# Optimization experiments

Hardware: AMD Instinct MI355X
Metric: run time of the kernel (lower is better)

Reference implementation:

```python
import jax, jax.numpy as jnp
import numpy as np

DIM = 768
NUM_HEADS = 12
HEAD_DIM = DIM // NUM_HEADS
B, N = 16, 784


def setup_inputs() -> dict:
    key = jax.random.key(0)
    k1, k2, k3, k4, k5 = jax.random.split(key, 5)
    x = jax.random.normal(k1, (B, N, DIM), dtype=jnp.float32)
    # Dense params (flax Dense: kernel [in, out], bias [out])
    Wqkv = jax.random.normal(k2, (DIM, 3 * DIM), dtype=jnp.float32) * (DIM ** -0.5)
    bqkv = jnp.zeros((3 * DIM,), dtype=jnp.float32)
    Wo = jax.random.normal(k3, (DIM, DIM), dtype=jnp.float32) * (DIM ** -0.5)
    bo = jnp.zeros((DIM,), dtype=jnp.float32)
    return {"x": x, "Wqkv": Wqkv, "bqkv": bqkv, "Wo": Wo, "bo": bo}


def reference(x, Wqkv, bqkv, Wo, bo):
    b, n, dim = x.shape
    # fused QKV projection
    qkv = jnp.einsum('bnd,df->bnf', x, Wqkv) + bqkv          # [b, n, 3*dim]
    qkv = qkv.reshape(b, n, 3, NUM_HEADS, HEAD_DIM)           # '(k h d)' split
    q, k, v = qkv[:, :, 0], qkv[:, :, 1], qkv[:, :, 2]        # [b, n, h, d]
    scale = HEAD_DIM ** -0.5
    # chunked/flash path computes exact softmax attention; same math, expressed densely
    scores = jnp.einsum('bihd,bjhd->bhij', q, k) * scale      # [b, h, n, n]
    attn = jax.nn.softmax(scores, axis=-1)
    out = jnp.einsum('bhij,bjhd->bihd', attn, v)              # [b, n, h, d]
    out = out.reshape(b, n, dim)                              # 'b n (h d)'
    return jnp.einsum('bnd,df->bnf', out, Wo) + bo
```

## Files before the change

kernel.cpp:

```cpp
#include <hip/hip_runtime.h>

#define DIM 768
#define NHEADS 12
#define HDIM 64
#define BB 16
#define NN 784
#define M_TOTAL (BB * NN)

typedef __attribute__((ext_vector_type(8))) _Float16 f16x8;
typedef __attribute__((ext_vector_type(4))) float f32x4;
typedef __attribute__((ext_vector_type(16))) float f32x16;
typedef __fp16 fp16x2 __attribute__((ext_vector_type(2)));

typedef __attribute__((address_space(3))) unsigned int lds_uint;
typedef __attribute__((address_space(1))) const unsigned int g_uint;
__device__ inline void gload_lds16(const void* g, void* l) {
    __builtin_amdgcn_global_load_lds((g_uint*)(uintptr_t)g,
                                     (lds_uint*)(uintptr_t)l, 16, 0, 0);
}

#if __has_builtin(__builtin_amdgcn_exp2f)
#define EXP2(x) __builtin_amdgcn_exp2f(x)
#else
#define EXP2(x) exp2f(x)
#endif

__device__ inline unsigned int pk2(float a, float b, float* lacc) {
#if __has_builtin(__builtin_amdgcn_cvt_pkrtz)
    union { fp16x2 h; unsigned int u; } r;
    r.h = __builtin_amdgcn_cvt_pkrtz(a, b);
#if __has_builtin(__builtin_amdgcn_fdot2)
    const fp16x2 one = {(__fp16)1.f, (__fp16)1.f};
    *lacc = __builtin_amdgcn_fdot2(r.h, one, *lacc, false);
#else
    *lacc += a + b;
#endif
    return r.u;
#else
    union { _Float16 h[2]; unsigned int u; } r;
    r.h[0] = (_Float16)a; r.h[1] = (_Float16)b;
    *lacc += a + b;
    return r.u;
#endif
}

__global__ __launch_bounds__(256) void prep_kernel(
    const float* __restrict__ x, _Float16* __restrict__ xh,
    const float* __restrict__ Wqkv, _Float16* __restrict__ wqT,
    const float* __restrict__ Wo, _Float16* __restrict__ woT)
{
    const int NC  = (M_TOTAL * DIM) / (8 * 256);
    const int NQX = (3 * DIM) / 32;
    const int NQ  = NQX * (DIM / 32);
    const int NOX = DIM / 32;
    const int bid = blockIdx.x;

    if (bid < NC) {
        const int i = (bid * 256 + threadIdx.x) * 8;
        float4 a = *(const float4*)&x[i];
        float4 b = *(const float4*)&x[i + 4];
        union { _Float16 h[8]; uint4 v; } o;
        o.h[0] = (_Float16)a.x; o.h[1] = (_Float16)a.y;
        o.h[2] = (_Float16)a.z; o.h[3] = (_Float16)a.w;
        o.h[4] = (_Float16)b.x; o.h[5] = (_Float16)b.y;
        o.h[6] = (_Float16)b.z; o.h[7] = (_Float16)b.w;
        *(uint4*)&xh[i] = o.v;
        return;
    }

    __shared__ float t[32][33];
    const float* W; _Float16* T; int N, n0, k0;
    if (bid < NC + NQ) {
        const int lb = bid - NC;
        W = Wqkv; T = wqT; N = 3 * DIM;
        n0 = (lb % NQX) * 32; k0 = (lb / NQX) * 32;
    } else {
        const int lb = bid - NC - NQ;
        W = Wo; T = woT; N = DIM;
        n0 = (lb % NOX) * 32; k0 = (lb / NOX) * 32;
    }
    const int K = DIM;
    const int r = threadIdx.x >> 3, c4 = (threadIdx.x & 7) * 4;
    float4 v = *(const float4*)&W[(size_t)(k0 + r) * N + n0 + c4];
    t[r][c4 + 0] = v.x; t[r][c4 + 1] = v.y;
    t[r][c4 + 2] = v.z; t[r][c4 + 3] = v.w;
    __syncthreads();
    union { _Float16 h[4]; ushort4 v4; } o;
#pragma unroll
    for (int i = 0; i < 4; ++i) o.h[i] = (_Float16)t[c4 + i][r];
    *(ushort4*)&T[(size_t)(n0 + r) * K + k0 + c4] = o.v4;
}

#define G_STAGE(BUF, K0)                                                       \
  {                                                                            \
    _Pragma("unroll")                                                          \
    for (int i = 0; i < 4; ++i) {                                              \
        const int rbase = w * 32 + i * 8;                                      \
        gload_lds16(A + (size_t)(gm + rbase + srow) * K + (K0) + scol,         \
                    &sA[BUF][rbase * 64]);                                     \
        gload_lds16(B + (size_t)(gn + rbase + srow) * K + (K0) + scol,         \
                    &sB[BUF][rbase * 64]);                                     \
    }                                                                          \
  }

#define G_COMPUTE(BUF)                                                         \
  {                                                                            \
    _Pragma("unroll")                                                          \
    for (int kk = 0; kk < 4; ++kk) {                                           \
        const int c = kk * 2 + hi;                                             \
        const int sw = (c ^ (l31 & 7)) * 8;                                    \
        f16x8 a[4], bb[2];                                                     \
        _Pragma("unroll")                                                      \
        for (int mt = 0; mt < 4; ++mt)                                         \
            a[mt] = *(const f16x8*)&sA[BUF][(wm + mt * 32 + l31) * 64 + sw];   \
        _Pragma("unroll")                                                      \
        for (int nt = 0; nt < 2; ++nt)                                         \
            bb[nt] = *(const f16x8*)&sB[BUF][(wn + nt * 32 + l31) * 64 + sw];  \
        __builtin_amdgcn_s_setprio(1);                                         \
        _Pragma("unroll")                                                      \
        for (int mt = 0; mt < 4; ++mt)                                         \
            _Pragma("unroll")                                                  \
            for (int nt = 0; nt < 2; ++nt)                                     \
                acc[mt][nt] = __builtin_amdgcn_mfma_f32_32x32x16_f16(          \
                    a[mt], bb[nt], acc[mt][nt], 0, 0, 0);                      \
        __builtin_amdgcn_s_setprio(0);                                         \
    }                                                                          \
  }

template <int OUT_F16>
__global__ __launch_bounds__(512) void gemm_f16_kernel(
    const _Float16* __restrict__ A, const _Float16* __restrict__ B,
    const float* __restrict__ bias, void* __restrict__ Cout,
    int M, int N, int K)
{
    __shared__ _Float16 sA[2][256 * 64];
    __shared__ _Float16 sB[2][256 * 64];

    const int tid  = threadIdx.x;
    const int w    = tid >> 6;
    const int lane = tid & 63;

    const int nwg = gridDim.x * gridDim.y;
    const int lid = blockIdx.x + gridDim.x * blockIdx.y;
    const int cq  = nwg >> 3, cr = nwg & 7;
    const int xcd = lid & 7, ix = lid >> 3;
    const int wgid = (xcd < cr ? xcd * (cq + 1) : cr * (cq + 1) + (xcd - cr) * cq) + ix;
    const int gn = (wgid % gridDim.x) * 256;
    const int gm = (wgid / gridDim.x) * 256;

    const int wm = (w & 1) * 128;
    const int wn = (w >> 1) * 64;
    const int l31 = lane & 31;
    const int hi  = lane >> 5;

    const int srow = lane >> 3;
    const int scol = ((lane & 7) ^ srow) * 8;

    f32x16 acc[4][2] = {};

    const int NT = K >> 6;
    G_STAGE(0, 0)
    __syncthreads();
    int cur = 0;
#pragma unroll 1
    for (int t = 0; t < NT - 1; ++t) {
        G_STAGE(cur ^ 1, (t + 1) * 64)
        G_COMPUTE(cur)
        __syncthreads();
        cur ^= 1;
    }
    G_COMPUTE(cur)

#pragma unroll
    for (int nt = 0; nt < 2; ++nt) {
        const int col = gn + wn + nt * 32 + l31;
        const float bv = bias[col];
#pragma unroll
        for (int mt = 0; mt < 4; ++mt) {
            f32x16 v = acc[mt][nt];
#pragma unroll
            for (int reg = 0; reg < 16; ++reg) {
                const int row = gm + wm + mt * 32 + (reg & 3) + 8 * (reg >> 2) + 4 * hi;
                const float o = v[reg] + bv;
                if (OUT_F16)
                    ((_Float16*)Cout)[(size_t)row * N + col] = (_Float16)o;
                else
                    ((float*)Cout)[(size_t)row * N + col] = o;
            }
        }
    }
}

#define LOG2E_8 0.18033688f

#define LOAD_TILE(J0, TAIL)                                                    \
  {                                                                            \
    const int j0_ = (J0);                                                      \
    int jrowK = j0_ + sj;                                                      \
    if (TAIL && jrowK > NN - 1) jrowK = NN - 1;                                \
    const size_t kbase = (size_t)(b * NN + jrowK) * (3 * DIM) + DIM + h * HDIM;\
    k0v = *(const uint4*)&qkv[kbase + sg * 8];                                 \
    k1v = *(const uint4*)&qkv[kbase + sg * 8 + 32];                            \
    int vr0 = j0_ + 2 * jj, vr1 = j0_ + 2 * jj + 1;                            \
    if (TAIL) { if (vr0 > NN - 1) vr0 = NN - 1; if (vr1 > NN - 1) vr1 = NN - 1; } \
    va.v = *(const uint4*)&qkv[(size_t)(b * NN + vr0) * (3 * DIM) + 2 * DIM + h * HDIM + dsub]; \
    vc.v = *(const uint4*)&qkv[(size_t)(b * NN + vr1) * (3 * DIM) + 2 * DIM + h * HDIM + dsub]; \
  }

#define WRITE_TILE(BUF)                                                        \
  {                                                                            \
    _Float16 (*K_)[72] = Ks[BUF];                                              \
    _Float16 (*V_)[72] = Vt[BUF];                                              \
    *(uint4*)&K_[sj][sg * 8]      = k0v;                                       \
    *(uint4*)&K_[sj][sg * 8 + 32] = k1v;                                       \
    _Pragma("unroll")                                                          \
    for (int i = 0; i < 8; ++i) {                                              \
        union { _Float16 h2[2]; unsigned int u; } t;                           \
        t.h2[0] = va.h[i]; t.h2[1] = vc.h[i];                                  \
        *(unsigned int*)&V_[dsub + i][pcol] = t.u;                             \
    }                                                                          \
  }

#define EXP_PACK(SV, G, J0_, TAIL)                                             \
  {                                                                            \
    float p0 = EXP2(SV[0]), p1 = EXP2(SV[1]);                                  \
    float p2 = EXP2(SV[2]), p3 = EXP2(SV[3]);                                  \
    if (TAIL && (J0_ + nt * 16) >= NN) { p0 = p1 = p2 = p3 = 0.f; }            \
    pk[G][nt][0] = pk2(p0, p1, &lpart[G]);                                     \
    pk[G][nt][1] = pk2(p2, p3, &lpart[G]);                                     \
  }

#define COMPUTE_TILE(BUF, J0, TAIL)                                            \
  {                                                                            \
    _Float16 (*K_)[72] = Ks[BUF];                                              \
    _Float16 (*V_)[72] = Vt[BUF];                                              \
    unsigned int pk[2][4][2];                                                  \
    _Pragma("unroll")                                                          \
    for (int nt = 0; nt < 4; ++nt) {                                           \
        f16x8 kf0 = *(const f16x8*)&K_[nt * 16 + l16][quad * 8];               \
        f16x8 kf1 = *(const f16x8*)&K_[nt * 16 + l16][32 + quad * 8];          \
        f32x4 s0 = {}, s1 = {};                                                \
        s0 = __builtin_amdgcn_mfma_f32_16x16x32_f16(kf0, qfrag[0][0], s0, 0, 0, 0); \
        s0 = __builtin_amdgcn_mfma_f32_16x16x32_f16(kf1, qfrag[0][1], s0, 0, 0, 0); \
        s1 = __builtin_amdgcn_mfma_f32_16x16x32_f16(kf0, qfrag[1][0], s1, 0, 0, 0); \
        s1 = __builtin_amdgcn_mfma_f32_16x16x32_f16(kf1, qfrag[1][1], s1, 0, 0, 0); \
        EXP_PACK(s0, 0, J0, TAIL)                                              \
        EXP_PACK(s1, 1, J0, TAIL)                                              \
    }                                                                          \
    __builtin_amdgcn_s_setprio(1);                                             \
    _Pragma("unroll")                                                          \
    for (int pc = 0; pc < 2; ++pc) {                                           \
        union { unsigned int u[4]; f16x8 v; } pa0, pa1;                        \
        pa0.u[0] = pk[0][2 * pc][0];     pa0.u[1] = pk[0][2 * pc][1];          \
        pa0.u[2] = pk[0][2 * pc + 1][0]; pa0.u[3] = pk[0][2 * pc + 1][1];      \
        pa1.u[0] = pk[1][2 * pc][0];     pa1.u[1] = pk[1][2 * pc][1];          \
        pa1.u[2] = pk[1][2 * pc + 1][0]; pa1.u[3] = pk[1][2 * pc + 1][1];      \
        _Pragma("unroll")                                                      \
        for (int dt = 0; dt < 4; ++dt) {                                       \
            f16x8 vf = *(const f16x8*)&V_[dt * 16 + l16][pc * 32 + quad * 8];  \
            O[0][dt] = __builtin_amdgcn_mfma_f32_16x16x32_f16(pa0.v, vf, O[0][dt], 0, 0, 0); \
            O[1][dt] = __builtin_amdgcn_mfma_f32_16x16x32_f16(pa1.v, vf, O[1][dt], 0, 0, 0); \
        }                                                                      \
    }                                                                          \
    __builtin_amdgcn_s_setprio(0);                                             \
  }

__global__ __launch_bounds__(256, 2) void attn_f16_kernel(
    const _Float16* __restrict__ qkv, _Float16* __restrict__ oat)
{
    const int L   = blockIdx.x + 7 * (blockIdx.y + NHEADS * blockIdx.z);
    const int xcd = L & 7, ixc = L >> 3;
    const int grp = xcd * 24 + ixc / 7;
    const int q0  = (ixc % 7) * 128;
    const int b   = grp / NHEADS;
    const int h   = grp % NHEADS;

    const int tid = threadIdx.x;
    const int wave = tid >> 6;
    const int lane = tid & 63;
    const int quad = lane >> 4;
    const int l16  = lane & 15;

    __shared__ _Float16 Ks[2][64][72];
    __shared__ _Float16 Vt[2][64][72];

    f16x8 qfrag[2][2];
#pragma unroll
    for (int g = 0; g < 2; ++g) {
        int qrow = q0 + wave * 32 + g * 16 + l16; if (qrow > NN - 1) qrow = NN - 1;
        size_t base = (size_t)(b * NN + qrow) * (3 * DIM) + h * HDIM;
        qfrag[g][0] = (*(const f16x8*)&qkv[base + quad * 8]) * (_Float16)LOG2E_8;
        qfrag[g][1] = (*(const f16x8*)&qkv[base + 32 + quad * 8]) * (_Float16)LOG2E_8;
    }

    const int sj = lane;
    const int sg = wave;
    const int jj   = lane & 31;
    const int dsub = sg * 16 + (lane >> 5) * 8;
    const int pcol = ((jj >> 4) << 5) | (((jj >> 1) & 3) << 3)
                   | (((jj >> 3) & 1) << 2) | ((jj & 1) << 1);

    f32x4 O[2][4] = {};
    float lpart[2] = {0.f, 0.f};

    uint4 k0v, k1v;
    union { uint4 v; _Float16 h[8]; } va, vc;

    LOAD_TILE(0, 0)
#pragma unroll 1
    for (int jt = 0; jt < 11; ++jt) {
        WRITE_TILE(jt & 1)
        __syncthreads();
        LOAD_TILE((jt + 1) * 64, 0)
        COMPUTE_TILE(jt & 1, 0, 0)
    }
    WRITE_TILE(1)
    __syncthreads();
    LOAD_TILE(768, 1)
    COMPUTE_TILE(1, 704, 0)
    WRITE_TILE(0)
    __syncthreads();
    COMPUTE_TILE(0, 768, 1)

#pragma unroll
    for (int g = 0; g < 2; ++g) {
        float t = lpart[g];
        t += __shfl_xor(t, 16);
        t += __shfl_xor(t, 32);
        float inv[4];
#pragma unroll
        for (int r = 0; r < 4; ++r)
            inv[r] = 1.0f / __shfl(t, quad * 4 + r, 16);
#pragma unroll
        for (int r = 0; r < 4; ++r) {
            const int q = q0 + wave * 32 + g * 16 + quad * 4 + r;
            if (q < NN) {
#pragma unroll
                for (int dt = 0; dt < 4; ++dt) {
                    const size_t base = (size_t)(b * NN + q) * DIM + h * HDIM + dt * 16 + l16;
                    oat[base] = (_Float16)(O[g][dt][r] * inv[r]);
                }
            }
        }
    }
}

extern "C" void kernel_launch(void* const* d_in, const int* in_sizes, int n_in,
                              void* d_out, int out_size, void* d_ws, size_t ws_size,
                              hipStream_t stream) {
    const float* x    = (const float*)d_in[0];
    const float* Wqkv = (const float*)d_in[1];
    const float* bqkv = (const float*)d_in[2];
    const float* Wo   = (const float*)d_in[3];
    const float* bo   = (const float*)d_in[4];
    float* out = (float*)d_out;

    _Float16* qkv = (_Float16*)d_ws;
    _Float16* xh  = qkv + (size_t)M_TOTAL * 3 * DIM;
    _Float16* wqT = xh + (size_t)M_TOTAL * DIM;
    _Float16* woT = wqT + (size_t)3 * DIM * DIM;
    _Float16* oat = xh;

    {
        const int NC = (M_TOTAL * DIM) / (8 * 256);
        const int NQ = ((3 * DIM) / 32) * (DIM / 32);
        const int NO_ = (DIM / 32) * (DIM / 32);
        prep_kernel<<<NC + NQ + NO_, 256, 0, stream>>>(
            x, xh, Wqkv, wqT, Wo, woT);
    }
    gemm_f16_kernel<1><<<dim3((3 * DIM) / 256, M_TOTAL / 256), 512, 0, stream>>>(
        xh, wqT, bqkv, qkv, M_TOTAL, 3 * DIM, DIM);
    attn_f16_kernel<<<dim3(7, NHEADS, BB), 256, 0, stream>>>(qkv, oat);
    gemm_f16_kernel<0><<<dim3(DIM / 256, M_TOTAL / 256), 512, 0, stream>>>(
        oat, woT, bo, out, M_TOTAL, DIM, DIM);
}
```

Before: 228.3 us.

## Interleave global-to-LDS loads with MFMA phases using fine-grained vmcnt waits

Restructures the double-buffered GEMM main loop so the next tile's B and A loads are issued in chunks between four MFMA phases. Each phase covers one 32-row A subtile, and explicit s_waitcnt vmcnt counts plus raw s_barrier replace __syncthreads. B fragments are held in registers across the whole k-tile and A is read per phase. The aim is to spread memory issue and hide load latency under matrix math. In exchange it carries more live registers and depends on fragile manual wait counts and buffer-reuse ordering, which could race.

New measurement: 226.0 us, median of 2. No clear change (-1.0%).

```diff
diff --git a/kernel.cpp b/kernel.cpp
--- a/kernel.cpp
+++ b/kernel.cpp
@@ -91,41 +91,43 @@
     *(ushort4*)&T[(size_t)(n0 + r) * K + k0 + c4] = o.v4;
 }
 
-#define G_STAGE(BUF, K0)                                                       \
-  {                                                                            \
-    _Pragma("unroll")                                                          \
-    for (int i = 0; i < 4; ++i) {                                              \
-        const int rbase = w * 32 + i * 8;                                      \
-        gload_lds16(A + (size_t)(gm + rbase + srow) * K + (K0) + scol,         \
-                    &sA[BUF][rbase * 64]);                                     \
-        gload_lds16(B + (size_t)(gn + rbase + srow) * K + (K0) + scol,         \
-                    &sB[BUF][rbase * 64]);                                     \
-    }                                                                          \
-  }
-
-#define G_COMPUTE(BUF)                                                         \
-  {                                                                            \
+#define VMCNT(N) asm volatile("s_waitcnt vmcnt(" #N ")" ::: "memory")
+#define BARRIER() { asm volatile("" ::: "memory"); \
+                    __builtin_amdgcn_s_barrier();  \
+                    asm volatile("" ::: "memory"); }
+
+#define ISSUE_A(BUF, K0, I)                                                    \
+    gload_lds16(A + (size_t)(gm + (I) * 64 + w * 8 + srow) * K + (K0) + scol,  \
+                &sA[BUF][((I) * 64 + w * 8) * 64]);
+#define ISSUE_B(BUF, K0, I)                                                    \
+    gload_lds16(B + (size_t)(gn + (I) * 64 + w * 8 + srow) * K + (K0) + scol,  \
+                &sB[BUF][((I) * 64 + w * 8) * 64]);
+
+#define READ_B()                                                               \
+  { _Pragma("unroll")                                                          \
+    for (int kk = 0; kk < 4; ++kk) {                                           \
+        const int sw = ((kk * 2 + hi) ^ (l31 & 7)) * 8;                        \
+        breg[0][kk] = *(const f16x8*)&sB[cur][(wn + l31) * 64 + sw];           \
+        breg[1][kk] = *(const f16x8*)&sB[cur][(wn + 32 + l31) * 64 + sw];      \
+    } }
+
+#define READ_A(P)                                                              \
+  { _Pragma("unroll")                                                          \
+    for (int kk = 0; kk < 4; ++kk) {                                           \
+        const int sw = ((kk * 2 + hi) ^ (l31 & 7)) * 8;                        \
+        af[kk] = *(const f16x8*)&sA[cur][(wm + (P) * 32 + l31) * 64 + sw];     \
+    } }
+
+#define MFMA_P(P)                                                              \
+  { __builtin_amdgcn_s_setprio(1);                                             \
     _Pragma("unroll")                                                          \
     for (int kk = 0; kk < 4; ++kk) {                                           \
-        const int c = kk * 2 + hi;                                             \
-        const int sw = (c ^ (l31 & 7)) * 8;                                    \
-        f16x8 a[4], bb[2];                                                     \
-        _Pragma("unroll")                                                      \
-        for (int mt = 0; mt < 4; ++mt)                                         \
-            a[mt] = *(const f16x8*)&sA[BUF][(wm + mt * 32 + l31) * 64 + sw];   \
-        _Pragma("unroll")                                                      \
-        for (int nt = 0; nt < 2; ++nt)                                         \
-            bb[nt] = *(const f16x8*)&sB[BUF][(wn + nt * 32 + l31) * 64 + sw];  \
-        __builtin_amdgcn_s_setprio(1);                                         \
-        _Pragma("unroll")                                                      \
-        for (int mt = 0; mt < 4; ++mt)                                         \
-            _Pragma("unroll")                                                  \
-            for (int nt = 0; nt < 2; ++nt)                                     \
-                acc[mt][nt] = __builtin_amdgcn_mfma_f32_32x32x16_f16(          \
-                    a[mt], bb[nt], acc[mt][nt], 0, 0, 0);                      \
-        __builtin_amdgcn_s_setprio(0);                                         \
+        acc[P][0] = __builtin_amdgcn_mfma_f32_32x32x16_f16(                    \
+            af[kk], breg[0][kk], acc[P][0], 0, 0, 0);                          \
+        acc[P][1] = __builtin_amdgcn_mfma_f32_32x32x16_f16(                    \
+            af[kk], breg[1][kk], acc[P][1], 0, 0, 0);                          \
     }                                                                          \
-  }
+    __builtin_amdgcn_s_setprio(0); }
 
 template <int OUT_F16>
 __global__ __launch_bounds__(512) void gemm_f16_kernel(
@@ -157,19 +159,39 @@
     const int scol = ((lane & 7) ^ srow) * 8;
 
     f32x16 acc[4][2] = {};
+    f16x8 breg[2][4], af[4];
 
     const int NT = K >> 6;
-    G_STAGE(0, 0)
-    __syncthreads();
+
+    ISSUE_B(0, 0, 0) ISSUE_B(0, 0, 1) ISSUE_B(0, 0, 2) ISSUE_B(0, 0, 3)
+    ISSUE_A(0, 0, 0) ISSUE_A(0, 0, 2) ISSUE_A(0, 0, 1) ISSUE_A(0, 0, 3)
+    VMCNT(2);
+    BARRIER();
+
     int cur = 0;
 #pragma unroll 1
-    for (int t = 0; t < NT - 1; ++t) {
-        G_STAGE(cur ^ 1, (t + 1) * 64)
-        G_COMPUTE(cur)
-        __syncthreads();
+    for (int t = 0; t < NT; ++t) {
+        const int kn = (t + 1) * 64;
+        const int nb = cur ^ 1;
+        const bool more = (t + 1 < NT);
+        if (more) { ISSUE_B(nb, kn, 0) ISSUE_B(nb, kn, 1) }
+        READ_B()
+        READ_A(0)
+        MFMA_P(0)
+        if (more) { ISSUE_B(nb, kn, 2) ISSUE_B(nb, kn, 3) }
+        READ_A(1)
+        MFMA_P(1)
+        if (more) { VMCNT(4); } else { VMCNT(0); }
+        BARRIER();
+        if (more) { ISSUE_A(nb, kn, 0) ISSUE_A(nb, kn, 2) }
+        READ_A(2)
+        MFMA_P(2)
+        if (more) { ISSUE_A(nb, kn, 1) ISSUE_A(nb, kn, 3) }
+        READ_A(3)
+        MFMA_P(3)
+        if (more) { VMCNT(2); BARRIER(); }
         cur ^= 1;
     }
-    G_COMPUTE(cur)
 
 #pragma unroll
     for (int nt = 0; nt < 2; ++nt) {
```
